# Performance work log

Measured on AMD Instinct MI355X. Metric: run time of the kernel, lower is better.

The kernel has to match this reference:

```python
import jax, jax.numpy as jnp
import numpy as np

B, N, M, DQ, DK, DV, H = 8, 1024, 1024, 512, 512, 512, 8
DH = DV // H           # per-head dim (dim_split)
DFF = 4 * DV           # FFN hidden dim
EPS = 1e-5


def _layernorm(x, g, b):
    mu = jnp.mean(x, axis=-1, keepdims=True)
    var = jnp.mean(jnp.square(x - mu), axis=-1, keepdims=True)
    return (x - mu) * jax.lax.rsqrt(var + EPS) * g + b


def setup_inputs() -> dict:
    key = jax.random.key(0)
    ks = jax.random.split(key, 20)
    s = 0.02
    return {
        "Q": jax.random.normal(ks[0], (B, N, DQ), jnp.float32),
        "K": jax.random.normal(ks[1], (B, M, DK), jnp.float32),
        "Wq": jax.random.normal(ks[2], (DV, DQ), jnp.float32) * s,
        "bq": jnp.zeros((DV,), jnp.float32),
        "Wk": jax.random.normal(ks[3], (DV, DK), jnp.float32) * s,
        "bk": jnp.zeros((DV,), jnp.float32),
        "Wv": jax.random.normal(ks[4], (DV, DK), jnp.float32) * s,
        "bv": jnp.zeros((DV,), jnp.float32),
        "W1": jax.random.normal(ks[5], (DFF, DV), jnp.float32) * s,
        "b1": jnp.zeros((DFF,), jnp.float32),
        "W2": jax.random.normal(ks[6], (DFF, DFF), jnp.float32) * s,
        "b2": jnp.zeros((DFF,), jnp.float32),
        "W3": jax.random.normal(ks[7], (DV, DFF), jnp.float32) * s,
        "b3": jnp.zeros((DV,), jnp.float32),
        "g0": jnp.ones((DV,), jnp.float32),
        "beta0": jnp.zeros((DV,), jnp.float32),
        "g1": jnp.ones((DV,), jnp.float32),
        "beta1": jnp.zeros((DV,), jnp.float32),
    }


def reference(Q, K, Wq, bq, Wk, bk, Wv, bv, W1, b1, W2, b2, W3, b3, g0, beta0, g1, beta1):
    # projections (torch Linear: x @ W.T + b)
    Qp = Q @ Wq.T + bq            # [B, N, DV]
    Kp = K @ Wk.T + bk            # [B, M, DV]
    Vp = K @ Wv.T + bv            # [B, M, DV]

    # split heads: [B, S, DV] -> [B, S, H, DH]
    Qh = Qp.reshape(B, N, H, DH)
    Kh = Kp.reshape(B, M, H, DH)
    Vh = Vp.reshape(B, M, H, DH)

    # scaled dot-product attention (scale = sqrt(head_dim))
    A = jnp.einsum("bnhd,bmhd->bhnm", Qh, Kh) / jnp.sqrt(jnp.float32(DH))
    A = jax.nn.softmax(A, axis=-1)
    O = jnp.einsum("bhnm,bmhd->bnhd", A, Vh).reshape(B, N, DV)

    # residual with projected Q, then LN
    O = _layernorm(O + Qp, g0, beta0)

    # FFN: Linear->ReLU->Linear->ReLU->Linear (num_hidden_layers=2)
    h = jax.nn.relu(O @ W1.T + b1)
    h = jax.nn.relu(h @ W2.T + b2)
    Off = h @ W3.T + b3

    return _layernorm(O + Off, g1, beta1)
```

## Files before the change

### kernel.cpp

```cpp
#include <hip/hip_runtime.h>


typedef __bf16 bf16_t;
typedef __bf16 bf16x8 __attribute__((ext_vector_type(8)));
typedef __bf16 bf16x4 __attribute__((ext_vector_type(4)));
typedef __bf16 bf16x2 __attribute__((ext_vector_type(2)));
typedef float  f32x4  __attribute__((ext_vector_type(4)));
typedef float  f32x16 __attribute__((ext_vector_type(16)));
typedef int    i32x4_t __attribute__((ext_vector_type(4)));
typedef int    i32x8_t __attribute__((ext_vector_type(8)));

__device__ __forceinline__ f32x4 mfma16(bf16x8 a, bf16x8 b, f32x4 c) {
  return __builtin_amdgcn_mfma_f32_16x16x32_bf16(a, b, c, 0, 0, 0);
}

__device__ __forceinline__ void gload_lds16(const void* g, void* l) {
  __builtin_amdgcn_global_load_lds((const __attribute__((address_space(1))) void*)g,
                                   (__attribute__((address_space(3))) void*)l,
                                   16, 0, 0);
}

__device__ __forceinline__ unsigned char to_fp8(float v) {
  return (unsigned char)(__builtin_amdgcn_cvt_pk_fp8_f32(v, v, 0, false) & 0xff);
}

__global__ __launch_bounds__(256) void cast_all(
    const float* __restrict__ Q, const float* __restrict__ K,
    const float* __restrict__ Wq, const float* __restrict__ Wk,
    const float* __restrict__ Wv, const float* __restrict__ W1,
    const float* __restrict__ W2, const float* __restrict__ W3,
    bf16_t* Qb, bf16_t* Kb, bf16_t* Wqb, bf16_t* Wkb, bf16_t* Wvb,
    bf16_t* W1b, unsigned char* W2q, bf16_t* W3b)
{
  long i = ((long)blockIdx.x * 256 + threadIdx.x) * 4;
  if (i >= 10223616L && i < 14417920L) {
    long o = i - 10223616L;
    float4 v = *(const float4*)(W2 + o);
    unsigned int lo = __builtin_amdgcn_cvt_pk_fp8_f32(v.x, v.y, 0, false);
    unsigned int hi = __builtin_amdgcn_cvt_pk_fp8_f32(v.z, v.w, 0, false);
    *(unsigned int*)(W2q + o) = (lo & 0xffffu) | (hi << 16);
    return;
  }
  const float* s; bf16_t* d; long o;
  if      (i <  4194304L) { s = Q;  d = Qb;  o = i;             }
  else if (i <  8388608L) { s = K;  d = Kb;  o = i - 4194304L;  }
  else if (i <  8650752L) { s = Wq; d = Wqb; o = i - 8388608L;  }
  else if (i <  8912896L) { s = Wk; d = Wkb; o = i - 8650752L;  }
  else if (i <  9175040L) { s = Wv; d = Wvb; o = i - 8912896L;  }
  else if (i < 10223616L) { s = W1; d = W1b; o = i - 9175040L;  }
  else                    { s = W3; d = W3b; o = i - 14417920L; }
  float4 v = *(const float4*)(s + o);
  bf16x4 w;
  w[0] = (bf16_t)v.x; w[1] = (bf16_t)v.y; w[2] = (bf16_t)v.z; w[3] = (bf16_t)v.w;
  *(bf16x4*)(d + o) = w;
}

template <int BM, bool RELU, bool VTEPI>
__device__ __forceinline__ void gemm_core(
    const bf16_t* __restrict__ A, const bf16_t* __restrict__ W,
    const float* __restrict__ bias, float* __restrict__ Cf,
    bf16_t* __restrict__ Cb, unsigned char* __restrict__ C8,
    bf16_t* __restrict__ VTout,
    float bscale, int N, int K, int lda, int ldb, int bx, int by)
{
  constexpr int WM = (BM == 128) ? 2 : 1;
  constexpr int WN = 4 / WM;
  constexpr int FI = 4;
  constexpr int FJ = 128 / (WN * 16);
  constexpr int CN = 128 / WN;
  constexpr int AISS = BM / 32;
  constexpr int SM_AB = (BM + 128) * 64 * 2;
  constexpr int SM_TS = 128 * 132 * 2;
  constexpr int SMEM = (VTEPI && SM_TS > SM_AB) ? SM_TS : SM_AB;

  __shared__ __align__(16) char smem[SMEM];
  bf16_t* As = (bf16_t*)smem;
  bf16_t* Bs = (bf16_t*)(smem + BM * 64 * 2);

  const int tid  = threadIdx.x;
  const int wave = tid >> 6, lane = tid & 63;
  const int lq   = lane & 15, quad = lane >> 4;
  const int wm   = (WM == 2) ? (wave & 1) : 0;
  const int wn   = (WM == 2) ? (wave >> 1) : wave;
  const long row0 = (long)bx * BM;
  const long col0 = (long)by * 128;

  const int sr = tid >> 3;
  const int cg = (tid & 7) ^ (sr & 7);
  const bf16_t* ag = A + (row0 + sr) * (long)lda + cg * 8;
  const bf16_t* bg = W + (col0 + sr) * (long)ldb + cg * 8;
  char* asD = (char*)As + wave * 1024;
  char* bsD = (char*)Bs + wave * 1024;

  const int off0 = (quad ^ (lq & 7)) * 8;
  const bf16_t* aR0 = As + (wm * 64 + lq) * 64 + off0;
  const bf16_t* aR1 = As + (wm * 64 + lq) * 64 + (off0 ^ 32);
  const bf16_t* bR0 = Bs + (wn * CN + lq) * 64 + off0;
  const bf16_t* bR1 = Bs + (wn * CN + lq) * 64 + (off0 ^ 32);

  f32x4 acc[FI][FJ];
#pragma unroll
  for (int i = 0; i < FI; i++)
#pragma unroll
    for (int j = 0; j < FJ; j++) acc[i][j] = (f32x4){0.f, 0.f, 0.f, 0.f};

  const long arows32 = 32L * lda;
  const long brows32 = 32L * ldb;
  for (int k0 = 0; k0 < K; k0 += 64) {
    __syncthreads();
#pragma unroll
    for (int is = 0; is < AISS; is++)
      gload_lds16(ag + is * arows32 + k0, asD + is * 4096);
#pragma unroll
    for (int is = 0; is < 4; is++)
      gload_lds16(bg + is * brows32 + k0, bsD + is * 4096);
    __syncthreads();
    bf16x8 af[FI], bw[FJ];
#pragma unroll
    for (int i = 0; i < FI; i++) af[i] = *(const bf16x8*)(aR0 + i * 1024);
#pragma unroll
    for (int j = 0; j < FJ; j++) bw[j] = *(const bf16x8*)(bR0 + j * 1024);
#pragma unroll
    for (int i = 0; i < FI; i++)
#pragma unroll
      for (int j = 0; j < FJ; j++)
        acc[i][j] = mfma16(af[i], bw[j], acc[i][j]);
#pragma unroll
    for (int i = 0; i < FI; i++) af[i] = *(const bf16x8*)(aR1 + i * 1024);
#pragma unroll
    for (int j = 0; j < FJ; j++) bw[j] = *(const bf16x8*)(bR1 + j * 1024);
#pragma unroll
    for (int i = 0; i < FI; i++)
#pragma unroll
      for (int j = 0; j < FJ; j++)
        acc[i][j] = mfma16(af[i], bw[j], acc[i][j]);
  }

  float bc[FJ];
#pragma unroll
  for (int j = 0; j < FJ; j++)
    bc[j] = bias ? bias[col0 + wn * CN + j * 16 + lq] : 0.f;

  if (VTEPI && VTout) {
    bf16_t* Ts = (bf16_t*)smem;
    __syncthreads();
#pragma unroll
    for (int i = 0; i < FI; i++)
#pragma unroll
      for (int j = 0; j < FJ; j++) {
        bf16x4 pv;
#pragma unroll
        for (int r = 0; r < 4; r++) pv[r] = (bf16_t)(acc[i][j][r] + bc[j]);
        *(bf16x4*)(Ts + (wn * CN + j * 16 + lq) * 132 + wm * 64 + i * 16 + quad * 4) = pv;
      }
    __syncthreads();
    const int b  = bx >> 3;
    const int mb = (bx & 7) * 128;
    const int h0 = by * 2;
    const int dd = tid >> 4;
    const int mc = (tid & 15) * 8;
#pragma unroll
    for (int p = 0; p < 8; p++) {
      const int d = dd + p * 16;
      bf16x8 v = *(const bf16x8*)(Ts + d * 132 + mc);
      *(bf16x8*)(VTout + ((long)(b * 8 + h0 + (d >> 6))) * 65536
                 + (d & 63) * 1024 + mb + mc) = v;
    }
    return;
  }

  const long rb = row0 + wm * 64 + quad * 4;
  const long cb = col0 + wn * CN + lq;
#pragma unroll
  for (int i = 0; i < FI; i++)
#pragma unroll
    for (int j = 0; j < FJ; j++)
#pragma unroll
      for (int r = 0; r < 4; r++) {
        float v = acc[i][j][r] + bc[j];
        if (RELU) v = fmaxf(v, 0.f);
        long idx = (rb + i * 16 + r) * (long)N + cb + j * 16;
        if (Cf) Cf[idx] = v;
        if (Cb) Cb[idx] = (bf16_t)(v * bscale);
        if (C8) C8[idx] = to_fp8(v);
      }
}

template <int BM, bool RELU>
__global__ __launch_bounds__(256) void gemm_bt(
    const bf16_t* __restrict__ A, const bf16_t* __restrict__ W,
    const float* __restrict__ bias, float* __restrict__ Cf,
    bf16_t* __restrict__ Cb, unsigned char* __restrict__ C8,
    float bscale, int N, int K)
{
  gemm_core<BM, RELU, false>(A, W, bias, Cf, Cb, C8, nullptr, bscale,
                             N, K, K, K, blockIdx.x, blockIdx.y);
}

__global__ __launch_bounds__(256) void ffn3_splitk(
    const bf16_t* __restrict__ H2, const bf16_t* __restrict__ W3b,
    bf16_t* __restrict__ Off01)
{
  const int z = blockIdx.z;
  gemm_core<128, false, false>(H2 + z * 1024, W3b + z * 1024, nullptr,
                               nullptr, Off01 + (long)z * 4194304, nullptr,
                               nullptr, 1.0f, 512, 1024, 2048, 2048,
                               blockIdx.x, blockIdx.y);
}

__global__ __launch_bounds__(256) void proj3(
    const bf16_t* __restrict__ Qb, const bf16_t* __restrict__ Kb,
    const bf16_t* __restrict__ Wqb, const bf16_t* __restrict__ Wkb,
    const bf16_t* __restrict__ Wvb,
    const float* __restrict__ bq, const float* __restrict__ bk,
    const float* __restrict__ bv,
    bf16_t* Qpb, bf16_t* Kpb, bf16_t* VT)
{
  const int z = blockIdx.z;
  const bf16_t* A  = (z == 0) ? Qb : Kb;
  const bf16_t* Wt = (z == 0) ? Wqb : ((z == 1) ? Wkb : Wvb);
  const float* bias = (z == 0) ? bq : ((z == 1) ? bk : bv);
  bf16_t* Cb = (z == 0) ? Qpb : ((z == 1) ? Kpb : nullptr);
  bf16_t* VTout = (z == 2) ? VT : nullptr;
  const float sc = (z == 1) ? 0.125f : 1.0f;
  gemm_core<128, false, true>(A, Wt, bias, nullptr, Cb, nullptr, VTout, sc,
                              512, 512, 512, 512, blockIdx.x, blockIdx.y);
}

__global__ __launch_bounds__(256) void ffn2_fp8(
    const unsigned char* __restrict__ H1, const unsigned char* __restrict__ W2,
    const float* __restrict__ bias, bf16_t* __restrict__ C)
{
  __shared__ unsigned char As[16384];
  __shared__ unsigned char Bs[16384];
  const int tid = threadIdx.x;
  const int wave = tid >> 6, lane = tid & 63;
  const int wm = wave & 1, wn = wave >> 1;
  const int m = lane & 31, h = lane >> 5;
  const long row0 = (long)blockIdx.x * 128;
  const long col0 = (long)blockIdx.y * 128;

  const int sr = tid >> 3;
  const int cg = (tid & 7) ^ (sr & 7);
  const unsigned char* ag = H1 + (row0 + sr) * 2048 + cg * 16;
  const unsigned char* bg = W2 + (col0 + sr) * 2048 + cg * 16;
  char* asD = (char*)As + wave * 1024;
  char* bsD = (char*)Bs + wave * 1024;

  const int ar0 = wm * 64 + m, ar1 = ar0 + 32;
  const int br0 = wn * 64 + m, br1 = br0 + 32;

  f32x16 acc[2][2];
#pragma unroll
  for (int mi = 0; mi < 2; mi++)
#pragma unroll
    for (int nj = 0; nj < 2; nj++)
#pragma unroll
      for (int r = 0; r < 16; r++) acc[mi][nj][r] = 0.f;

  for (int k0 = 0; k0 < 2048; k0 += 128) {
    __syncthreads();
#pragma unroll
    for (int is = 0; is < 4; is++)
      gload_lds16(ag + is * 65536 + k0, asD + is * 4096);
#pragma unroll
    for (int is = 0; is < 4; is++)
      gload_lds16(bg + is * 65536 + k0, bsD + is * 4096);
    __syncthreads();
#pragma unroll
    for (int ks = 0; ks < 2; ks++) {
      const int c0 = ks * 4 + h * 2;
      i32x8_t a[2], b[2];
#pragma unroll
      for (int mi = 0; mi < 2; mi++) {
        const int r = mi ? ar1 : ar0;
        i32x4_t lo = *(const i32x4_t*)(As + r * 128 + ((c0    ) ^ (r & 7)) * 16);
        i32x4_t hi = *(const i32x4_t*)(As + r * 128 + ((c0 + 1) ^ (r & 7)) * 16);
        a[mi][0] = lo[0]; a[mi][1] = lo[1]; a[mi][2] = lo[2]; a[mi][3] = lo[3];
        a[mi][4] = hi[0]; a[mi][5] = hi[1]; a[mi][6] = hi[2]; a[mi][7] = hi[3];
      }
#pragma unroll
      for (int nj = 0; nj < 2; nj++) {
        const int r = nj ? br1 : br0;
        i32x4_t lo = *(const i32x4_t*)(Bs + r * 128 + ((c0    ) ^ (r & 7)) * 16);
        i32x4_t hi = *(const i32x4_t*)(Bs + r * 128 + ((c0 + 1) ^ (r & 7)) * 16);
        b[nj][0] = lo[0]; b[nj][1] = lo[1]; b[nj][2] = lo[2]; b[nj][3] = lo[3];
        b[nj][4] = hi[0]; b[nj][5] = hi[1]; b[nj][6] = hi[2]; b[nj][7] = hi[3];
      }
#pragma unroll
      for (int mi = 0; mi < 2; mi++)
#pragma unroll
        for (int nj = 0; nj < 2; nj++)
          acc[mi][nj] = __builtin_amdgcn_mfma_scale_f32_32x32x64_f8f6f4(
              a[mi], b[nj], acc[mi][nj], 0, 0,
              0, 0x7f7f7f7f, 0, 0x7f7f7f7f);
    }
  }

  float bc[2];
  bc[0] = bias[col0 + wn * 64 + m];
  bc[1] = bias[col0 + wn * 64 + 32 + m];
#pragma unroll
  for (int mi = 0; mi < 2; mi++)
#pragma unroll
    for (int nj = 0; nj < 2; nj++)
#pragma unroll
      for (int reg = 0; reg < 16; reg++) {
        const int rl = (reg & 3) + 8 * (reg >> 2) + 4 * h;
        float v = fmaxf(acc[mi][nj][reg] + bc[nj], 0.f);
        C[(row0 + wm * 64 + mi * 32 + rl) * 2048 + col0 + wn * 64 + nj * 32 + m]
            = (bf16_t)v;
      }
}

__global__ __launch_bounds__(256) void attn(
    const bf16_t* __restrict__ Qp, const bf16_t* __restrict__ Kp,
    const bf16_t* __restrict__ VT, bf16_t* __restrict__ O)
{
  const int qb = blockIdx.x, h = blockIdx.y, b = blockIdx.z;
  const int tid = threadIdx.x;
  const int wave = tid >> 6, lane = tid & 63;
  const int lq = lane & 15, quad = lane >> 4;

  __shared__ bf16_t Ks[8192];
  __shared__ bf16_t VTs[8192];
  __shared__ bf16_t Ps[4][16 * 72];

  const long bh = (long)b * 1024;
  const int qrow = qb * 64 + wave * 16 + lq;

  const bf16_t* qptr = Qp + (bh + qrow) * 512 + h * 64 + quad * 8;
  const bf16x8 qf0 = *(const bf16x8*)qptr;
  const bf16x8 qf1 = *(const bf16x8*)(qptr + 32);

  f32x4 oacc[4];
#pragma unroll
  for (int t = 0; t < 4; t++) oacc[t] = (f32x4){0.f, 0.f, 0.f, 0.f};
  float l_i = 0.f;

  const int sr = tid >> 3;
  const int cg = (tid & 7) ^ (sr & 7);
  char* ksDst = (char*)Ks + wave * 1024;
  char* vtDst = (char*)VTs + wave * 1024;
  const bf16_t* kg  = Kp + bh * 512 + h * 64;
  const bf16_t* vtg = VT + ((long)b * 8 + h) * 65536;
  const int off0 = (quad ^ (lq & 7)) * 8;

  for (int m0 = 0; m0 < 1024; m0 += 128) {
    __syncthreads();
#pragma unroll
    for (int s = 0; s < 2; s++) {
      gload_lds16(kg + (long)(m0 + s * 64 + sr) * 512 + cg * 8,      ksDst + s * 8192);
      gload_lds16(kg + (long)(m0 + s * 64 + sr + 32) * 512 + cg * 8, ksDst + s * 8192 + 4096);
      gload_lds16(vtg + (long)sr * 1024 + m0 + s * 64 + cg * 8,        vtDst + s * 8192);
      gload_lds16(vtg + (long)(sr + 32) * 1024 + m0 + s * 64 + cg * 8, vtDst + s * 8192 + 4096);
    }
    __syncthreads();

    f32x4 st[8];
#pragma unroll
    for (int t = 0; t < 8; t++) {
      const bf16_t* kb = Ks + (t >> 2) * 4096 + ((t & 3) * 16 + lq) * 64;
      bf16x8 ka0 = *(const bf16x8*)(kb + off0);
      bf16x8 ka1 = *(const bf16x8*)(kb + (off0 ^ 32));
      f32x4 s = (f32x4){0.f, 0.f, 0.f, 0.f};
      s = mfma16(ka0, qf0, s);
      s = mfma16(ka1, qf1, s);
      st[t] = s;
    }
    float lsum = 0.f;
#pragma unroll
    for (int t = 0; t < 8; t++)
#pragma unroll
      for (int r = 0; r < 4; r++) {
        float p = __expf(st[t][r]);
        st[t][r] = p;
        lsum += p;
      }
    lsum += __shfl_xor(lsum, 16, 64);
    lsum += __shfl_xor(lsum, 32, 64);
    l_i += lsum;

    bf16_t* pw = &Ps[wave][0];
#pragma unroll
    for (int hh = 0; hh < 2; hh++) {
#pragma unroll
      for (int t = 0; t < 4; t++) {
        bf16x4 pv;
#pragma unroll
        for (int r = 0; r < 4; r++) pv[r] = (bf16_t)st[hh * 4 + t][r];
        *(bf16x4*)(pw + lq * 72 + t * 16 + quad * 4) = pv;
      }
#pragma unroll
      for (int ks = 0; ks < 2; ks++) {
        bf16x8 pb = *(const bf16x8*)(pw + lq * 72 + ks * 32 + quad * 8);
#pragma unroll
        for (int dt = 0; dt < 4; dt++) {
          const bf16_t* vb = VTs + hh * 4096 + (dt * 16 + lq) * 64;
          bf16x8 va = *(const bf16x8*)(vb + (ks ? (off0 ^ 32) : off0));
          oacc[dt] = mfma16(va, pb, oacc[dt]);
        }
      }
    }
  }

  const float inv = 1.f / l_i;
  bf16_t* op = O + (bh + qrow) * 512 + h * 64 + quad * 4;
#pragma unroll
  for (int dt = 0; dt < 4; dt++) {
    bf16x4 v;
#pragma unroll
    for (int r = 0; r < 4; r++) v[r] = (bf16_t)(oacc[dt][r] * inv);
    *(bf16x4*)(op + dt * 16) = v;
  }
}

__device__ __forceinline__ float2 ld2(const float* p, long row, int tid) {
  return ((const float2*)(p + row * 512))[tid];
}
__device__ __forceinline__ float2 ld2(const bf16_t* p, long row, int tid) {
  bf16x2 v = *(const bf16x2*)(p + row * 512 + tid * 2);
  return make_float2((float)v[0], (float)v[1]);
}

__device__ __forceinline__ void ln_finish(
    float x0, float x1, const float* g, const float* be, int tid,
    int wave, int lane, float* of, bf16_t* ob, long row)
{
  float s = x0 + x1, ss = x0 * x0 + x1 * x1;
#pragma unroll
  for (int off = 1; off < 64; off <<= 1) {
    s  += __shfl_xor(s,  off, 64);
    ss += __shfl_xor(ss, off, 64);
  }
  __shared__ float sm[8];
  if (lane == 0) { sm[wave] = s; sm[4 + wave] = ss; }
  __syncthreads();
  s  = sm[0] + sm[1] + sm[2] + sm[3];
  ss = sm[4] + sm[5] + sm[6] + sm[7];
  const float mu = s * (1.f / 512.f);
  const float var = ss * (1.f / 512.f) - mu * mu;
  const float rs = rsqrtf(var + 1e-5f);
  const float2 gg = ((const float2*)g)[tid];
  const float2 bb = ((const float2*)be)[tid];
  const float o0 = (x0 - mu) * rs * gg.x + bb.x;
  const float o1 = (x1 - mu) * rs * gg.y + bb.y;
  if (of) ((float2*)(of + row * 512))[tid] = make_float2(o0, o1);
  if (ob) {
    bf16x2 t; t[0] = (bf16_t)o0; t[1] = (bf16_t)o1;
    *(bf16x2*)(ob + row * 512 + tid * 2) = t;
  }
}

__global__ __launch_bounds__(256) void ln_res(
    const bf16_t* __restrict__ A, const bf16_t* __restrict__ Bv,
    const float* __restrict__ g, const float* __restrict__ be,
    bf16_t* __restrict__ ob)
{
  const int row = blockIdx.x, tid = threadIdx.x;
  const float2 va = ld2(A,  (long)row, tid);
  const float2 vb = ld2(Bv, (long)row, tid);
  ln_finish(va.x + vb.x, va.y + vb.y, g, be, tid, tid >> 6, tid & 63,
            nullptr, ob, row);
}

__global__ __launch_bounds__(256) void ln_res3(
    const bf16_t* __restrict__ X, const bf16_t* __restrict__ O0,
    const bf16_t* __restrict__ O1, const float* __restrict__ bias,
    const float* __restrict__ g, const float* __restrict__ be,
    float* __restrict__ of)
{
  const int row = blockIdx.x, tid = threadIdx.x;
  const float2 vx = ld2(X,  (long)row, tid);
  const float2 v0 = ld2(O0, (long)row, tid);
  const float2 v1 = ld2(O1, (long)row, tid);
  const float2 vb = ((const float2*)bias)[tid];
  ln_finish(vx.x + v0.x + v1.x + vb.x, vx.y + v0.y + v1.y + vb.y,
            g, be, tid, tid >> 6, tid & 63, of, nullptr, row);
}

extern "C" void kernel_launch(void* const* d_in, const int* in_sizes, int n_in,
                              void* d_out, int out_size, void* d_ws, size_t ws_size,
                              hipStream_t stream)
{
  const float* Q   = (const float*)d_in[0];
  const float* K   = (const float*)d_in[1];
  const float* Wq  = (const float*)d_in[2];
  const float* bq  = (const float*)d_in[3];
  const float* Wk  = (const float*)d_in[4];
  const float* bk  = (const float*)d_in[5];
  const float* Wv  = (const float*)d_in[6];
  const float* bv  = (const float*)d_in[7];
  const float* W1  = (const float*)d_in[8];
  const float* b1  = (const float*)d_in[9];
  const float* W2  = (const float*)d_in[10];
  const float* b2  = (const float*)d_in[11];
  const float* W3  = (const float*)d_in[12];
  const float* b3  = (const float*)d_in[13];
  const float* g0  = (const float*)d_in[14];
  const float* be0 = (const float*)d_in[15];
  const float* g1  = (const float*)d_in[16];
  const float* be1 = (const float*)d_in[17];

  char* ws = (char*)d_ws;
  bf16_t* Wqb = (bf16_t*)(ws + 0);
  bf16_t* Wkb = (bf16_t*)(ws + 524288);
  bf16_t* Wvb = (bf16_t*)(ws + 1048576);
  bf16_t* W1b = (bf16_t*)(ws + 1572864);
  bf16_t* W3b = (bf16_t*)(ws + 3670016);
  unsigned char* W2q = (unsigned char*)(ws + 5767168);
  bf16_t* Qb  = (bf16_t*)(ws + 14155776);
  bf16_t* Kb  = (bf16_t*)(ws + 22544384);
  bf16_t* Qpb = (bf16_t*)(ws + 30932992);
  bf16_t* Kpb = (bf16_t*)(ws + 39321600);
  bf16_t* VT  = (bf16_t*)(ws + 47710208);
  bf16_t* Of  = (bf16_t*)(ws + 14155776);
  bf16_t* Xb  = (bf16_t*)(ws + 22544384);
  bf16_t* H2  = (bf16_t*)(ws + 30932992);
  unsigned char* H1q = (unsigned char*)(ws + 64487424);
  bf16_t* Off0 = (bf16_t*)(ws + 64487424);
  bf16_t* Off1 = (bf16_t*)(ws + 72876032);
  float*  out = (float*)d_out;

  cast_all<<<15104, 256, 0, stream>>>(Q, K, Wq, Wk, Wv, W1, W2, W3,
                                      Qb, Kb, Wqb, Wkb, Wvb, W1b, W2q, W3b);
  proj3<<<dim3(64, 4, 3), 256, 0, stream>>>(Qb, Kb, Wqb, Wkb, Wvb, bq, bk, bv,
                                            Qpb, Kpb, VT);
  attn<<<dim3(16, 8, 8), 256, 0, stream>>>(Qpb, Kpb, VT, Of);
  ln_res<<<8192, 256, 0, stream>>>(Of, Qpb, g0, be0, Xb);
  gemm_bt<128, true ><<<dim3(64, 16), 256, 0, stream>>>(Xb, W1b, b1, nullptr, nullptr, H1q, 1.0f, 2048, 512);
  ffn2_fp8<<<dim3(64, 16), 256, 0, stream>>>(H1q, W2q, b2, H2);
  ffn3_splitk<<<dim3(64, 4, 2), 256, 0, stream>>>(H2, W3b, Off0);
  ln_res3<<<8192, 256, 0, stream>>>(Xb, Off0, Off1, b3, g1, be1, out);
}
```

Before: 293.0 us.

## Register-prefetch K/V tiles in attention and reorder blocks by batch-head

The attention kernel now loads each K/V tile into registers one iteration ahead and stores it to LDS after the barrier, replacing the direct global-to-LDS loads. The tile shrinks from 128 to 64 keys, which halves LDS use and so may let more blocks share a compute unit. The grid is flattened so consecutive blocks cover different batch-heads, which changes the order in which K/V data is reused through cache. The cost is more barriers per key pass and extra register pressure from the prefetch buffers.

```diff
diff --git a/kernel.cpp b/kernel.cpp
--- a/kernel.cpp
+++ b/kernel.cpp
@@ -317,19 +317,21 @@
     const bf16_t* __restrict__ Qp, const bf16_t* __restrict__ Kp,
     const bf16_t* __restrict__ VT, bf16_t* __restrict__ O)
 {
-  const int qb = blockIdx.x, h = blockIdx.y, b = blockIdx.z;
+  const int idx = blockIdx.x;
+  const int bh = idx & 63;
+  const int qb = idx >> 6;
+  const int b = bh >> 3, h = bh & 7;
   const int tid = threadIdx.x;
   const int wave = tid >> 6, lane = tid & 63;
   const int lq = lane & 15, quad = lane >> 4;
 
-  __shared__ bf16_t Ks[8192];
-  __shared__ bf16_t VTs[8192];
+  __shared__ bf16_t Ks[4096];
+  __shared__ bf16_t VTs[4096];
   __shared__ bf16_t Ps[4][16 * 72];
 
-  const long bh = (long)b * 1024;
+  const long bhl = (long)b * 1024;
   const int qrow = qb * 64 + wave * 16 + lq;
-
-  const bf16_t* qptr = Qp + (bh + qrow) * 512 + h * 64 + quad * 8;
+  const bf16_t* qptr = Qp + (bhl + qrow) * 512 + h * 64 + quad * 8;
   const bf16x8 qf0 = *(const bf16x8*)qptr;
   const bf16x8 qf1 = *(const bf16x8*)(qptr + 32);
 
@@ -338,31 +340,47 @@
   for (int t = 0; t < 4; t++) oacc[t] = (f32x4){0.f, 0.f, 0.f, 0.f};
   float l_i = 0.f;
 
-  const int sr = tid >> 3;
-  const int cg = (tid & 7) ^ (sr & 7);
-  char* ksDst = (char*)Ks + wave * 1024;
-  char* vtDst = (char*)VTs + wave * 1024;
-  const bf16_t* kg  = Kp + bh * 512 + h * 64;
-  const bf16_t* vtg = VT + ((long)b * 8 + h) * 65536;
-  const int off0 = (quad ^ (lq & 7)) * 8;
-
-  for (int m0 = 0; m0 < 1024; m0 += 128) {
-    __syncthreads();
-#pragma unroll
-    for (int s = 0; s < 2; s++) {
-      gload_lds16(kg + (long)(m0 + s * 64 + sr) * 512 + cg * 8,      ksDst + s * 8192);
-      gload_lds16(kg + (long)(m0 + s * 64 + sr + 32) * 512 + cg * 8, ksDst + s * 8192 + 4096);
-      gload_lds16(vtg + (long)sr * 1024 + m0 + s * 64 + cg * 8,        vtDst + s * 8192);
-      gload_lds16(vtg + (long)(sr + 32) * 1024 + m0 + s * 64 + cg * 8, vtDst + s * 8192 + 4096);
+  const int sr = tid >> 3, slot = tid & 7;
+  const int cg = slot ^ (sr & 7);
+  const bf16_t* kg  = Kp + bhl * 512 + h * 64;
+  const bf16_t* vtg = VT + (long)bh * 65536;
+  const bf16_t* kp0 = kg + (long)sr * 512 + cg * 8;
+  const bf16_t* kp1 = kg + (long)(sr + 32) * 512 + cg * 8;
+  const bf16_t* vp0 = vtg + (long)sr * 1024 + cg * 8;
+  const bf16_t* vp1 = vtg + (long)(sr + 32) * 1024 + cg * 8;
+
+  bf16x8 rk0 = *(const bf16x8*)kp0;
+  bf16x8 rk1 = *(const bf16x8*)kp1;
+  bf16x8 rv0 = *(const bf16x8*)vp0;
+  bf16x8 rv1 = *(const bf16x8*)vp1;
+
+  bf16_t* ksW0 = Ks  + sr * 64 + slot * 8;
+  bf16_t* ksW1 = Ks  + (sr + 32) * 64 + slot * 8;
+  bf16_t* vtW0 = VTs + sr * 64 + slot * 8;
+  bf16_t* vtW1 = VTs + (sr + 32) * 64 + slot * 8;
+
+  for (int it = 0; it < 16; it++) {
+    __syncthreads();
+    *(bf16x8*)ksW0 = rk0;
+    *(bf16x8*)ksW1 = rk1;
+    *(bf16x8*)vtW0 = rv0;
+    *(bf16x8*)vtW1 = rv1;
+    if (it < 15) {
+      kp0 += 64 * 512; kp1 += 64 * 512; vp0 += 64; vp1 += 64;
+      rk0 = *(const bf16x8*)kp0;
+      rk1 = *(const bf16x8*)kp1;
+      rv0 = *(const bf16x8*)vp0;
+      rv1 = *(const bf16x8*)vp1;
     }
     __syncthreads();
 
-    f32x4 st[8];
-#pragma unroll
-    for (int t = 0; t < 8; t++) {
-      const bf16_t* kb = Ks + (t >> 2) * 4096 + ((t & 3) * 16 + lq) * 64;
-      bf16x8 ka0 = *(const bf16x8*)(kb + off0);
-      bf16x8 ka1 = *(const bf16x8*)(kb + (off0 ^ 32));
+    f32x4 st[4];
+#pragma unroll
+    for (int t = 0; t < 4; t++) {
+      const int mloc = t * 16 + lq;
+      const int offK = (quad ^ (mloc & 7)) * 8;
+      bf16x8 ka0 = *(const bf16x8*)(Ks + mloc * 64 + offK);
+      bf16x8 ka1 = *(const bf16x8*)(Ks + mloc * 64 + (offK ^ 32));
       f32x4 s = (f32x4){0.f, 0.f, 0.f, 0.f};
       s = mfma16(ka0, qf0, s);
       s = mfma16(ka1, qf1, s);
@@ -370,7 +388,7 @@
     }
     float lsum = 0.f;
 #pragma unroll
-    for (int t = 0; t < 8; t++)
+    for (int t = 0; t < 4; t++)
 #pragma unroll
       for (int r = 0; r < 4; r++) {
         float p = __expf(st[t][r]);
@@ -383,29 +401,28 @@
 
     bf16_t* pw = &Ps[wave][0];
 #pragma unroll
-    for (int hh = 0; hh < 2; hh++) {
-#pragma unroll
-      for (int t = 0; t < 4; t++) {
-        bf16x4 pv;
-#pragma unroll
-        for (int r = 0; r < 4; r++) pv[r] = (bf16_t)st[hh * 4 + t][r];
-        *(bf16x4*)(pw + lq * 72 + t * 16 + quad * 4) = pv;
-      }
-#pragma unroll
-      for (int ks = 0; ks < 2; ks++) {
-        bf16x8 pb = *(const bf16x8*)(pw + lq * 72 + ks * 32 + quad * 8);
-#pragma unroll
-        for (int dt = 0; dt < 4; dt++) {
-          const bf16_t* vb = VTs + hh * 4096 + (dt * 16 + lq) * 64;
-          bf16x8 va = *(const bf16x8*)(vb + (ks ? (off0 ^ 32) : off0));
-          oacc[dt] = mfma16(va, pb, oacc[dt]);
-        }
-      }
+    for (int t = 0; t < 4; t++) {
+      bf16x4 pv;
+#pragma unroll
+      for (int r = 0; r < 4; r++) pv[r] = (bf16_t)st[t][r];
+      *(bf16x4*)(pw + lq * 72 + t * 16 + quad * 4) = pv;
     }
+
+#pragma unroll
+    for (int ks = 0; ks < 2; ks++) {
+      bf16x8 pb = *(const bf16x8*)(pw + lq * 72 + ks * 32 + quad * 8);
+#pragma unroll
+      for (int dt = 0; dt < 4; dt++) {
+        const int row = dt * 16 + lq;
+        const int offV = (quad ^ (row & 7)) * 8;
+        bf16x8 va = *(const bf16x8*)(VTs + row * 64 + (ks ? (offV ^ 32) : offV));
+        oacc[dt] = mfma16(va, pb, oacc[dt]);
+      }
+    }
   }
 
   const float inv = 1.f / l_i;
-  bf16_t* op = O + (bh + qrow) * 512 + h * 64 + quad * 4;
+  bf16_t* op = O + (bhl + qrow) * 512 + h * 64 + quad * 4;
 #pragma unroll
   for (int dt = 0; dt < 4; dt++) {
     bf16x4 v;
@@ -526,7 +543,7 @@
                                       Qb, Kb, Wqb, Wkb, Wvb, W1b, W2q, W3b);
   proj3<<<dim3(64, 4, 3), 256, 0, stream>>>(Qb, Kb, Wqb, Wkb, Wvb, bq, bk, bv,
                                             Qpb, Kpb, VT);
-  attn<<<dim3(16, 8, 8), 256, 0, stream>>>(Qpb, Kpb, VT, Of);
+  attn<<<1024, 256, 0, stream>>>(Qpb, Kpb, VT, Of);
   ln_res<<<8192, 256, 0, stream>>>(Of, Qpb, g0, be0, Xb);
   gemm_bt<128, true ><<<dim3(64, 16), 256, 0, stream>>>(Xb, W1b, b1, nullptr, nullptr, H1q, 1.0f, 2048, 512);
   ffn2_fp8<<<dim3(64, 16), 256, 0, stream>>>(H1q, W2q, b2, H2);
```

New measurement: 294.2 us. No clear change (+0.4%).
